# Optimization experiments

Hardware: AMD Instinct MI355X
Metric: run time of the kernel (lower is better)

The kernel has to match this reference:

```python
import jax, jax.numpy as jnp
import numpy as np
import math

N_NODES = 50000
N_EDGES = 800000
IN_FEATS = 128
HID = 64
OUT = 2
D = 2  # num_layers


def calc_thetas(d):
    """Beta-distribution polynomial coefficients (ascending order), matching
    sympy.poly((x/2)**i * (1-x/2)**(d-i) / Beta(i+1, d+1-i)) with inverted coeffs."""
    thetas = []
    for i in range(d + 1):
        p1 = np.zeros(i + 1)
        p1[-1] = 0.5 ** i  # (x/2)^i, ascending coeffs
        p2 = np.array([math.comb(d - i, j) * (-0.5) ** j for j in range(d - i + 1)])  # (1-x/2)^(d-i)
        beta = math.factorial(i) * math.factorial(d - i) / math.factorial(d + 1)
        thetas.append((np.convolve(p1, p2) / beta).tolist())
    return thetas


def poly_branch(h, src, dst, thetas):
    """Run all PolyConv filters on activated features h; concat along feature dim."""
    n = h.shape[0]
    deg = jnp.zeros((n,), h.dtype).at[dst].add(jnp.ones((dst.shape[0],), h.dtype))
    dinv = jnp.clip(deg, 1.0, None) ** -0.5  # D^{-1/2} of in-degrees, clamped min 1
    dinv = dinv[:, None]
    outs = []
    for th in thetas:
        f = h
        acc = th[0] * h
        for k in range(1, len(th)):
            # feat <- feat - D^{-1/2} A D^{-1/2} feat  (copy_u / sum aggregation)
            agg = jax.ops.segment_sum((f * dinv)[src], dst, num_segments=n)
            f = f - agg * dinv
            acc = acc + th[k] * f
        outs.append(acc)
    return jnp.concatenate(outs, axis=-1)


def setup_inputs() -> dict:
    key = jax.random.key(0)
    ks = jax.random.split(key, 12)
    inp = {
        "x": jax.random.normal(ks[0], (N_NODES, IN_FEATS), jnp.float32),
        "sim_x": jax.random.normal(ks[1], (N_NODES, IN_FEATS), jnp.float32),
        "src": jax.random.randint(ks[2], (N_EDGES,), 0, N_NODES, jnp.int32),
        "dst": jax.random.randint(ks[3], (N_EDGES,), 0, N_NODES, jnp.int32),
        "sim_src": jax.random.randint(ks[4], (N_EDGES,), 0, N_NODES, jnp.int32),
        "sim_dst": jax.random.randint(ks[5], (N_EDGES,), 0, N_NODES, jnp.int32),
        "W1_o": jax.random.normal(ks[6], (IN_FEATS, HID), jnp.float32) / np.sqrt(IN_FEATS),
        "b1_o": jnp.zeros((HID,), jnp.float32),
        "W1_s": jax.random.normal(ks[7], (IN_FEATS, HID), jnp.float32) / np.sqrt(IN_FEATS),
        "b1_s": jnp.zeros((HID,), jnp.float32),
        "Wm1": jax.random.normal(ks[8], (HID * (D + 1) * 2, HID), jnp.float32) / np.sqrt(HID * (D + 1) * 2),
        "bm1": jnp.zeros((HID,), jnp.float32),
        "Wm2": jax.random.normal(ks[9], (HID, OUT), jnp.float32) / np.sqrt(HID),
        "bm2": jnp.zeros((OUT,), jnp.float32),
    }
    return inp


def reference(x, sim_x, src, dst, sim_src, sim_dst,
              W1_o, b1_o, W1_s, b1_s, Wm1, bm1, Wm2, bm2):
    thetas_o = calc_thetas(D)
    thetas_s = [[4.0] * (D + 1) for _ in range(D + 1)]  # conv_s uses constant theta=4

    h = jax.nn.relu(x @ W1_o + b1_o)
    h_final = poly_branch(h, src, dst, thetas_o)      # [N, HID*(D+1)]

    sh = jax.nn.relu(sim_x @ W1_s + b1_s)
    sim_h_final = poly_branch(sh, sim_src, sim_dst, thetas_s)

    h_all = jnp.concatenate([h_final, sim_h_final], axis=-1)  # [N, HID*(D+1)*2]
    logits = jax.nn.relu(h_all @ Wm1 + bm1) @ Wm2 + bm2
    return (h_all, logits)
```

## Files before the change

### kernel.cpp

```cpp
#include <hip/hip_runtime.h>
#include <hip/hip_fp16.h>


#define KB_BITS 10
#define KMAX 64
#define PCHUNK 4096
#define PVPT 16

__global__ __launch_bounds__(256) void bhist_kernel(
    const int* __restrict__ dst, const int* __restrict__ sim_dst,
    int* __restrict__ bhist, int E, int Es) {
    __shared__ int h[2 * KMAX];
    int tid = threadIdx.x;
    if (tid < 2 * KMAX) h[tid] = 0;
    __syncthreads();
    int total = E + Es;
    for (int e = blockIdx.x * 256 + tid; e < total; e += gridDim.x * 256) {
        if (e < E) atomicAdd(&h[dst[e] >> KB_BITS], 1);
        else       atomicAdd(&h[KMAX + (sim_dst[e - E] >> KB_BITS)], 1);
    }
    __syncthreads();
    if (tid < 2 * KMAX && h[tid]) atomicAdd(&bhist[tid], h[tid]);
}

__global__ __launch_bounds__(128) void bscan_kernel(
    const int* __restrict__ bhist, int* __restrict__ brow,
    int* __restrict__ gcur) {
    int g = threadIdx.x >> 6, lane = threadIdx.x & 63;
    int v = bhist[g * KMAX + lane];
    int inc = v;
    #pragma unroll
    for (int off = 1; off < 64; off <<= 1) {
        int u = __shfl_up(inc, off);
        if (lane >= off) inc += u;
    }
    int ex = inc - v;
    brow[g * (KMAX + 1) + lane] = ex;
    if (lane == 63) brow[g * (KMAX + 1) + KMAX] = inc;
    gcur[g * KMAX + lane] = ex;
}

__global__ __launch_bounds__(256) void partition_kernel(
    const int* __restrict__ src, const int* __restrict__ dst,
    const int* __restrict__ sim_src, const int* __restrict__ sim_dst,
    int* __restrict__ gcur, unsigned* __restrict__ staged,
    int E, int Es, int nbo) {
    int b = blockIdx.x;
    const int* S; const int* D; int Eg; int goff; unsigned* stg;
    if (b < nbo) { S = src; D = dst; Eg = E; goff = 0; stg = staged; }
    else { b -= nbo; S = sim_src; D = sim_dst; Eg = Es; goff = KMAX; stg = staged + E; }
    int e0 = b * PCHUNK;
    int cnt_blk = Eg - e0; if (cnt_blk > PCHUNK) cnt_blk = PCHUNK;
    __shared__ int hist[KMAX], basep[KMAX], cur[KMAX], gbase[KMAX];
    __shared__ unsigned srt[PCHUNK];
    int tid = threadIdx.x;
    if (tid < KMAX) hist[tid] = 0;
    __syncthreads();
    unsigned full[PVPT];
    #pragma unroll
    for (int i = 0; i < PVPT; ++i) {
        int idx = i * 256 + tid;
        if (idx < cnt_blk) {
            int e = e0 + idx;
            int d = D[e];
            unsigned bk = (unsigned)d >> KB_BITS;
            full[i] = (bk << 26) | ((unsigned)S[e] << KB_BITS) |
                      (unsigned)(d & ((1 << KB_BITS) - 1));
            atomicAdd(&hist[bk], 1);
        } else full[i] = 0xFFFFFFFFu;
    }
    __syncthreads();
    if (tid < 64) {
        int v = hist[tid];
        int inc = v;
        #pragma unroll
        for (int off = 1; off < 64; off <<= 1) {
            int u = __shfl_up(inc, off);
            if (tid >= off) inc += u;
        }
        int ex = inc - v;
        basep[tid] = ex;
        cur[tid] = ex;
        gbase[tid] = v ? atomicAdd(&gcur[goff + tid], v) : 0;
    }
    __syncthreads();
    #pragma unroll
    for (int i = 0; i < PVPT; ++i) {
        unsigned f = full[i];
        if (f != 0xFFFFFFFFu) {
            unsigned bk = f >> 26;
            int slot = atomicAdd(&cur[bk], 1);
            srt[slot] = f;
        }
    }
    __syncthreads();
    for (int slot = tid; slot < cnt_blk; slot += 256) {
        unsigned f = srt[slot];
        unsigned bk = f >> 26;
        int gpos = gbase[bk] + (slot - basep[bk]);
        stg[gpos] = f & 0x3FFFFFFu;
    }
}

__global__ __launch_bounds__(512) void place_kernel(
    const unsigned* __restrict__ staged, const int* __restrict__ brow,
    int* __restrict__ row_o, int* __restrict__ row_s,
    int* __restrict__ esrc_o, int* __restrict__ esrc_s,
    float* __restrict__ dinv, int N, int K, int E) {
    int b = blockIdx.x;
    const unsigned* stg; const int* br; int* row; int* esrc; float* dv;
    if (b < K) { stg = staged; br = brow; row = row_o; esrc = esrc_o; dv = dinv; }
    else { b -= K; stg = staged + E; br = brow + (KMAX + 1); row = row_s; esrc = esrc_s; dv = dinv + N; }
    int node0 = b << KB_BITS;
    int nn = N - node0; if (nn > (1 << KB_BITS)) nn = (1 << KB_BITS);
    int seg0 = br[b], seg1 = br[b + 1];
    __shared__ int ncnt[1 << KB_BITS];
    __shared__ int wsum[8];
    int tid = threadIdx.x;
    for (int i = tid; i < (1 << KB_BITS); i += 512) ncnt[i] = 0;
    __syncthreads();
    for (int j = seg0 + tid; j < seg1; j += 512)
        atomicAdd(&ncnt[stg[j] & ((1 << KB_BITS) - 1)], 1);
    __syncthreads();
    int i0 = tid * 2;
    int v0 = ncnt[i0], v1 = ncnt[i0 + 1];
    int s = v0 + v1;
    int inc = s;
    #pragma unroll
    for (int off = 1; off < 64; off <<= 1) {
        int u = __shfl_up(inc, off);
        if ((tid & 63) >= off) inc += u;
    }
    if ((tid & 63) == 63) wsum[tid >> 6] = inc;
    __syncthreads();
    int wo = 0;
    for (int w = 0; w < (tid >> 6); ++w) wo += wsum[w];
    int ex = seg0 + wo + inc - s;
    if (i0 < nn) {
        row[node0 + i0] = ex;
        dv[node0 + i0] = rsqrtf((float)(v0 > 1 ? v0 : 1));
    }
    if (i0 + 1 < nn) {
        row[node0 + i0 + 1] = ex + v0;
        dv[node0 + i0 + 1] = rsqrtf((float)(v1 > 1 ? v1 : 1));
    }
    if (b == K - 1 && tid == 0) row[N] = br[K];
    __syncthreads();
    ncnt[i0] = ex;
    ncnt[i0 + 1] = ex + v0;
    __syncthreads();
    for (int j = seg0 + tid; j < seg1; j += 512) {
        unsigned f = stg[j];
        int pos = atomicAdd(&ncnt[f & ((1 << KB_BITS) - 1)], 1);
        esrc[pos] = (int)(f >> KB_BITS);
    }
}

__global__ __launch_bounds__(256) void fold_kernel(
    const float* __restrict__ Wm1, float* __restrict__ w1f) {
    int i = blockIdx.x * 256 + threadIdx.x;
    if (i >= 256 * 64) return;
    int k = i >> 6, j = i & 63;
    float v = Wm1[k * 64 + j];
    if (k >= 192) v += Wm1[(k + 64) * 64 + j] + Wm1[(k + 128) * 64 + j];
    w1f[i] = v;
}

__global__ __launch_bounds__(256) void in_gemm2_kernel(
    const float* __restrict__ x, const float* __restrict__ sim_x,
    const float* __restrict__ W1_o, const float* __restrict__ b1_o,
    const float* __restrict__ W1_s, const float* __restrict__ b1_s,
    float* __restrict__ hall, __half* __restrict__ h16_o, __half* __restrict__ h16_s,
    const float* __restrict__ dinv, int n, int nbh, int f16path) {
    int bb = blockIdx.x;
    const float* xin; const float* W; const float* b; __half* h16;
    const float* dinvv; int off;
    if (bb < nbh) { xin = x; W = W1_o; b = b1_o; h16 = h16_o; dinvv = dinv; off = 0; }
    else { bb -= nbh; xin = sim_x; W = W1_s; b = b1_s; h16 = h16_s; dinvv = dinv + n; off = 192; }
    __shared__ float xs[64][132];
    __shared__ float Wf[128][68];
    int tid = threadIdx.x;
    int node0 = bb * 64;
    const float4* wsrc = (const float4*)W;
    for (int i = tid; i < 2048; i += 256)
        *(float4*)&Wf[i >> 4][(i & 15) * 4] = wsrc[i];
    const float4* xsrc = (const float4*)xin;
    for (int i = tid; i < 2048; i += 256) {
        int nl = i >> 5, c = i & 31;
        int node = node0 + nl;
        float4 v = make_float4(0.f, 0.f, 0.f, 0.f);
        if (node < n) v = xsrc[(long)node * 32 + c];
        *(float4*)&xs[nl][c * 4] = v;
    }
    __syncthreads();
    int tx = tid & 15, ty = tid >> 4;
    float acc[4][4] = {};
    #pragma unroll 2
    for (int k = 0; k < 128; k += 4) {
        float4 a[4], bbv[4];
        #pragma unroll
        for (int i = 0; i < 4; ++i) a[i] = *(const float4*)&xs[ty * 4 + i][k];
        #pragma unroll
        for (int j = 0; j < 4; ++j) bbv[j] = *(const float4*)&Wf[k + j][tx * 4];
        #pragma unroll
        for (int i = 0; i < 4; ++i) {
            acc[i][0] = fmaf(a[i].x, bbv[0].x, acc[i][0]);
            acc[i][1] = fmaf(a[i].x, bbv[0].y, acc[i][1]);
            acc[i][2] = fmaf(a[i].x, bbv[0].z, acc[i][2]);
            acc[i][3] = fmaf(a[i].x, bbv[0].w, acc[i][3]);
            acc[i][0] = fmaf(a[i].y, bbv[1].x, acc[i][0]);
            acc[i][1] = fmaf(a[i].y, bbv[1].y, acc[i][1]);
            acc[i][2] = fmaf(a[i].y, bbv[1].z, acc[i][2]);
            acc[i][3] = fmaf(a[i].y, bbv[1].w, acc[i][3]);
            acc[i][0] = fmaf(a[i].z, bbv[2].x, acc[i][0]);
            acc[i][1] = fmaf(a[i].z, bbv[2].y, acc[i][1]);
            acc[i][2] = fmaf(a[i].z, bbv[2].z, acc[i][2]);
            acc[i][3] = fmaf(a[i].z, bbv[2].w, acc[i][3]);
            acc[i][0] = fmaf(a[i].w, bbv[3].x, acc[i][0]);
            acc[i][1] = fmaf(a[i].w, bbv[3].y, acc[i][1]);
            acc[i][2] = fmaf(a[i].w, bbv[3].z, acc[i][2]);
            acc[i][3] = fmaf(a[i].w, bbv[3].w, acc[i][3]);
        }
    }
    float4 bias = *(const float4*)&b[tx * 4];
    #pragma unroll
    for (int i = 0; i < 4; ++i) {
        int node = node0 + ty * 4 + i;
        if (node >= n) break;
        float4 r;
        r.x = fmaxf(acc[i][0] + bias.x, 0.0f);
        r.y = fmaxf(acc[i][1] + bias.y, 0.0f);
        r.z = fmaxf(acc[i][2] + bias.z, 0.0f);
        r.w = fmaxf(acc[i][3] + bias.w, 0.0f);
        if (f16path) {
            float dvn = dinvv[node];
            __half hh[4];
            hh[0] = __float2half_rn(r.x * dvn);
            hh[1] = __float2half_rn(r.y * dvn);
            hh[2] = __float2half_rn(r.z * dvn);
            hh[3] = __float2half_rn(r.w * dvn);
            *(float2*)&h16[(long)node * 64 + tx * 4] = *(float2*)hh;
        } else {
            *(float4*)&hall[(long)node * 384 + off + tx * 4] = r;
        }
    }
}

__global__ __launch_bounds__(256) void hop1_kernel(
    const int* __restrict__ row_o, const int* __restrict__ esrc_o,
    const int* __restrict__ row_s, const int* __restrict__ esrc_s,
    const __half* __restrict__ h16_o, const __half* __restrict__ h16_s,
    __half* __restrict__ g16_o, __half* __restrict__ g16_s,
    int n, int nb) {
    int b = blockIdx.x;
    const int* row; const int* esrc; const __half* h16; __half* g16;
    if (b < nb) { row = row_o; esrc = esrc_o; h16 = h16_o; g16 = g16_o; }
    else { b -= nb; row = row_s; esrc = esrc_s; h16 = h16_s; g16 = g16_s; }
    int d = b * 4 + (threadIdx.x >> 6);
    if (d >= n) return;
    int lane = threadIdx.x & 63;
    int p = row[d], end = row[d + 1];
    int deg = end - p;
    float degf = (float)(deg > 1 ? deg : 1);
    float dd = rsqrtf(degf);
    float h16v = __half2float(h16[(long)d * 64 + lane]);
    float a0 = 0.f, a1 = 0.f, a2 = 0.f, a3 = 0.f;
    for (; p + 16 <= end; p += 16) {
        int ss[16];
        #pragma unroll
        for (int i = 0; i < 16; ++i) ss[i] = esrc[p + i];
        #pragma unroll
        for (int i = 0; i < 16; i += 4) {
            a0 += __half2float(h16[(long)ss[i] * 64 + lane]);
            a1 += __half2float(h16[(long)ss[i + 1] * 64 + lane]);
            a2 += __half2float(h16[(long)ss[i + 2] * 64 + lane]);
            a3 += __half2float(h16[(long)ss[i + 3] * 64 + lane]);
        }
    }
    for (; p + 4 <= end; p += 4) {
        int s0 = esrc[p], s1 = esrc[p + 1], s2 = esrc[p + 2], s3 = esrc[p + 3];
        a0 += __half2float(h16[(long)s0 * 64 + lane]);
        a1 += __half2float(h16[(long)s1 * 64 + lane]);
        a2 += __half2float(h16[(long)s2 * 64 + lane]);
        a3 += __half2float(h16[(long)s3 * 64 + lane]);
    }
    for (; p < end; ++p) {
        int s = esrc[p];
        a0 += __half2float(h16[(long)s * 64 + lane]);
    }
    float acc = (a0 + a1) + (a2 + a3);
    g16[(long)d * 64 + lane] = __float2half_rn(h16v - acc * dd * dd);
}

__global__ __launch_bounds__(256) void hop2_kernel(
    const int* __restrict__ row_o, const int* __restrict__ esrc_o,
    const int* __restrict__ row_s, const int* __restrict__ esrc_s,
    const __half* __restrict__ h16_o, const __half* __restrict__ h16_s,
    const __half* __restrict__ g16_o, const __half* __restrict__ g16_s,
    float* __restrict__ hall, int n, int nb) {
    int b = blockIdx.x;
    int g = (b < nb) ? 0 : 1;
    const int* row; const int* esrc; const __half* h16; const __half* g16;
    if (g == 0) { row = row_o; esrc = esrc_o; h16 = h16_o; g16 = g16_o; }
    else { b -= nb; row = row_s; esrc = esrc_s; h16 = h16_s; g16 = g16_s; }
    int d = b * 4 + (threadIdx.x >> 6);
    if (d >= n) return;
    int lane = threadIdx.x & 63;
    int p = row[d], end = row[d + 1];
    int deg = end - p;
    float degf = (float)(deg > 1 ? deg : 1);
    float dd = rsqrtf(degf);
    float sq = sqrtf(degf);
    float f0 = __half2float(h16[(long)d * 64 + lane]) * sq;
    float f1 = __half2float(g16[(long)d * 64 + lane]) * sq;
    float a0 = 0.f, a1 = 0.f, a2 = 0.f, a3 = 0.f;
    for (; p + 16 <= end; p += 16) {
        int ss[16];
        #pragma unroll
        for (int i = 0; i < 16; ++i) ss[i] = esrc[p + i];
        #pragma unroll
        for (int i = 0; i < 16; i += 4) {
            a0 += __half2float(g16[(long)ss[i] * 64 + lane]);
            a1 += __half2float(g16[(long)ss[i + 1] * 64 + lane]);
            a2 += __half2float(g16[(long)ss[i + 2] * 64 + lane]);
            a3 += __half2float(g16[(long)ss[i + 3] * 64 + lane]);
        }
    }
    for (; p + 4 <= end; p += 4) {
        int s0 = esrc[p], s1 = esrc[p + 1], s2 = esrc[p + 2], s3 = esrc[p + 3];
        a0 += __half2float(g16[(long)s0 * 64 + lane]);
        a1 += __half2float(g16[(long)s1 * 64 + lane]);
        a2 += __half2float(g16[(long)s2 * 64 + lane]);
        a3 += __half2float(g16[(long)s3 * 64 + lane]);
    }
    for (; p < end; ++p) {
        int s = esrc[p];
        a0 += __half2float(g16[(long)s * 64 + lane]);
    }
    float acc = (a0 + a1) + (a2 + a3);
    float f2 = f1 - acc * dd;
    long ob = (long)d * 384 + lane;
    if (g == 0) {
        hall[ob]       = 3.0f * f0 - 3.0f * f1 + 0.75f * f2;
        hall[ob + 64]  = 3.0f * f1 - 1.5f * f2;
        hall[ob + 128] = 0.75f * f2;
    } else {
        float ss = 4.0f * (f0 + f1 + f2);
        hall[ob + 192] = ss; hall[ob + 256] = ss; hall[ob + 320] = ss;
    }
}

__global__ __launch_bounds__(256) void gather2_kernel(
    const int* __restrict__ row_o, const int* __restrict__ esrc_o, const float* __restrict__ dinv_o,
    const int* __restrict__ row_s, const int* __restrict__ esrc_s, const float* __restrict__ dinv_s,
    float* __restrict__ hall, int in_off_o, int in_off_s, int n, int nb) {
    int b = blockIdx.x;
    const int* row; const int* esrc; const float* dinv; int in_off;
    if (b < nb) { row = row_o; esrc = esrc_o; dinv = dinv_o; in_off = in_off_o; }
    else { b -= nb; row = row_s; esrc = esrc_s; dinv = dinv_s; in_off = in_off_s; }
    int d = b * 4 + (threadIdx.x >> 6);
    if (d >= n) return;
    int lane = threadIdx.x & 63;
    int p = row[d], end = row[d + 1];
    const float* fin = hall + in_off;
    float a0 = 0.f, a1 = 0.f, a2 = 0.f, a3 = 0.f;
    for (; p + 4 <= end; p += 4) {
        int s0 = esrc[p], s1 = esrc[p + 1], s2 = esrc[p + 2], s3 = esrc[p + 3];
        a0 = fmaf(fin[(long)s0 * 384 + lane], dinv[s0], a0);
        a1 = fmaf(fin[(long)s1 * 384 + lane], dinv[s1], a1);
        a2 = fmaf(fin[(long)s2 * 384 + lane], dinv[s2], a2);
        a3 = fmaf(fin[(long)s3 * 384 + lane], dinv[s3], a3);
    }
    for (; p < end; ++p) {
        int s = esrc[p];
        a0 = fmaf(fin[(long)s * 384 + lane], dinv[s], a0);
    }
    float acc = (a0 + a1) + (a2 + a3);
    long ob = (long)d * 384 + lane;
    hall[ob + in_off + 64] = fin[ob] - acc * dinv[d];
}

__global__ __launch_bounds__(256) void combine_kernel(float* __restrict__ h, int nf) {
    int i = blockIdx.x * 256 + threadIdx.x;
    if (i >= nf) return;
    long ob = (long)(i >> 6) * 384 + (i & 63);
    float f0v = h[ob], f1v = h[ob + 64], f2v = h[ob + 128];
    h[ob]       = 3.0f * f0v - 3.0f * f1v + 0.75f * f2v;
    h[ob + 64]  = 3.0f * f1v - 1.5f * f2v;
    h[ob + 128] = 0.75f * f2v;
    float ss = 4.0f * (h[ob + 192] + h[ob + 256] + h[ob + 320]);
    h[ob + 192] = ss; h[ob + 256] = ss; h[ob + 320] = ss;
}

__global__ __launch_bounds__(256) void mlp_kernel(
    const float* __restrict__ hall, const float* __restrict__ w1f,
    const float* __restrict__ bm1, const float* __restrict__ Wm2,
    const float* __restrict__ bm2, float* __restrict__ logits, int n) {
    __shared__ float xs[64][132];
    __shared__ float Wf[128][68];
    int tid = threadIdx.x;
    int node0 = blockIdx.x * 64;
    int tx = tid & 15, ty = tid >> 4;
    float acc[4][4] = {};
    const float4* wsrc = (const float4*)w1f;
    const float4* hsrc = (const float4*)hall;
    for (int c = 0; c < 2; ++c) {
        __syncthreads();
        for (int i = tid; i < 2048; i += 256)
            *(float4*)&Wf[i >> 4][(i & 15) * 4] = wsrc[c * 2048 + i];
        for (int i = tid; i < 2048; i += 256) {
            int nl = i >> 5, cc = i & 31;
            int node = node0 + nl;
            float4 v = make_float4(0.f, 0.f, 0.f, 0.f);
            if (node < n) v = hsrc[(long)node * 96 + c * 32 + cc];
            *(float4*)&xs[nl][cc * 4] = v;
        }
        __syncthreads();
        #pragma unroll 2
        for (int k = 0; k < 128; k += 4) {
            float4 a[4], bb[4];
            #pragma unroll
            for (int i = 0; i < 4; ++i) a[i] = *(const float4*)&xs[ty * 4 + i][k];
            #pragma unroll
            for (int j = 0; j < 4; ++j) bb[j] = *(const float4*)&Wf[k + j][tx * 4];
            #pragma unroll
            for (int i = 0; i < 4; ++i) {
                acc[i][0] = fmaf(a[i].x, bb[0].x, acc[i][0]);
                acc[i][1] = fmaf(a[i].x, bb[0].y, acc[i][1]);
                acc[i][2] = fmaf(a[i].x, bb[0].z, acc[i][2]);
                acc[i][3] = fmaf(a[i].x, bb[0].w, acc[i][3]);
                acc[i][0] = fmaf(a[i].y, bb[1].x, acc[i][0]);
                acc[i][1] = fmaf(a[i].y, bb[1].y, acc[i][1]);
                acc[i][2] = fmaf(a[i].y, bb[1].z, acc[i][2]);
                acc[i][3] = fmaf(a[i].y, bb[1].w, acc[i][3]);
                acc[i][0] = fmaf(a[i].z, bb[2].x, acc[i][0]);
                acc[i][1] = fmaf(a[i].z, bb[2].y, acc[i][1]);
                acc[i][2] = fmaf(a[i].z, bb[2].z, acc[i][2]);
                acc[i][3] = fmaf(a[i].z, bb[2].w, acc[i][3]);
                acc[i][0] = fmaf(a[i].w, bb[3].x, acc[i][0]);
                acc[i][1] = fmaf(a[i].w, bb[3].y, acc[i][1]);
                acc[i][2] = fmaf(a[i].w, bb[3].z, acc[i][2]);
                acc[i][3] = fmaf(a[i].w, bb[3].w, acc[i][3]);
            }
        }
    }
    __syncthreads();
    float4 bias = *(const float4*)&bm1[tx * 4];
    #pragma unroll
    for (int i = 0; i < 4; ++i) {
        xs[ty * 4 + i][tx * 4 + 0] = fmaxf(acc[i][0] + bias.x, 0.0f);
        xs[ty * 4 + i][tx * 4 + 1] = fmaxf(acc[i][1] + bias.y, 0.0f);
        xs[ty * 4 + i][tx * 4 + 2] = fmaxf(acc[i][2] + bias.z, 0.0f);
        xs[ty * 4 + i][tx * 4 + 3] = fmaxf(acc[i][3] + bias.w, 0.0f);
    }
    __syncthreads();
    if (tid < 128) {
        int nl = tid >> 1, o = tid & 1;
        int node = node0 + nl;
        if (node < n) {
            float p = bm2[o];
            #pragma unroll 8
            for (int k = 0; k < 64; ++k) p = fmaf(xs[nl][k], Wm2[k * 2 + o], p);
            logits[(long)node * 2 + o] = p;
        }
    }
}

extern "C" void kernel_launch(void* const* d_in, const int* in_sizes, int n_in,
                              void* d_out, int out_size, void* d_ws, size_t ws_size,
                              hipStream_t stream) {
    const float* x     = (const float*)d_in[0];
    const float* sim_x = (const float*)d_in[1];
    const int* src     = (const int*)d_in[2];
    const int* dst     = (const int*)d_in[3];
    const int* sim_src = (const int*)d_in[4];
    const int* sim_dst = (const int*)d_in[5];
    const float* W1_o = (const float*)d_in[6];
    const float* b1_o = (const float*)d_in[7];
    const float* W1_s = (const float*)d_in[8];
    const float* b1_s = (const float*)d_in[9];
    const float* Wm1  = (const float*)d_in[10];
    const float* bm1  = (const float*)d_in[11];
    const float* Wm2  = (const float*)d_in[12];
    const float* bm2  = (const float*)d_in[13];

    const int N  = in_sizes[0] / 128;
    const int E  = in_sizes[2];
    const int Es = in_sizes[4];
    const int NF = N * 64;
    const int K  = (N + (1 << KB_BITS) - 1) >> KB_BITS;

    float* hall = (float*)d_out;
    float* lgt  = hall + (long)N * 384;
    float* dinv = lgt;
    float* dinv_o = dinv;
    float* dinv_s = dinv + N;

    int* row_o  = (int*)d_ws;
    int* row_s  = row_o + (N + 1);
    int* esrc_o = row_s + (N + 1);
    int* esrc_s = esrc_o + E;
    int* bhist  = esrc_s + Es;
    int* brow   = bhist + 2 * KMAX;
    int* gcur   = brow + 2 * (KMAX + 1);
    float* w1f  = (float*)(gcur + 2 * KMAX);
    __half* h16_o = (__half*)(w1f + 256 * 64);
    __half* h16_s = h16_o + (long)N * 64;
    __half* g16_o = h16_s + (long)N * 64;
    __half* g16_s = g16_o + (long)N * 64;
    size_t need_f16 = (size_t)((char*)(g16_s + (long)N * 64) - (char*)d_ws);
    bool f16path = ws_size >= need_f16;
    unsigned* staged = (unsigned*)h16_o;

    int nb4  = (N + 3) / 4;
    int nb64 = (N + 63) / 64;
    int nfb  = (NF + 255) / 256;
    int nbo  = (E + PCHUNK - 1) / PCHUNK;
    int nbs  = (Es + PCHUNK - 1) / PCHUNK;

    hipMemsetAsync(bhist, 0, (size_t)(2 * KMAX) * sizeof(int), stream);
    fold_kernel<<<64, 256, 0, stream>>>(Wm1, w1f);
    bhist_kernel<<<256, 256, 0, stream>>>(dst, sim_dst, bhist, E, Es);
    bscan_kernel<<<1, 128, 0, stream>>>(bhist, brow, gcur);
    partition_kernel<<<nbo + nbs, 256, 0, stream>>>(src, dst, sim_src, sim_dst,
                                                    gcur, staged, E, Es, nbo);
    place_kernel<<<2 * K, 512, 0, stream>>>(staged, brow, row_o, row_s,
                                            esrc_o, esrc_s, dinv, N, K, E);

    in_gemm2_kernel<<<2 * nb64, 256, 0, stream>>>(x, sim_x, W1_o, b1_o, W1_s, b1_s,
                                                  hall, h16_o, h16_s, dinv, N, nb64,
                                                  f16path ? 1 : 0);

    if (f16path) {
        hop1_kernel<<<2 * nb4, 256, 0, stream>>>(row_o, esrc_o, row_s, esrc_s,
                                                 h16_o, h16_s, g16_o, g16_s, N, nb4);
        hop2_kernel<<<2 * nb4, 256, 0, stream>>>(row_o, esrc_o, row_s, esrc_s,
                                                 h16_o, h16_s, g16_o, g16_s,
                                                 hall, N, nb4);
    } else {
        gather2_kernel<<<2 * nb4, 256, 0, stream>>>(row_o, esrc_o, dinv_o,
                                                    row_s, esrc_s, dinv_s,
                                                    hall, 0, 192, N, nb4);
        gather2_kernel<<<2 * nb4, 256, 0, stream>>>(row_o, esrc_o, dinv_o,
                                                    row_s, esrc_s, dinv_s,
                                                    hall, 64, 256, N, nb4);
        combine_kernel<<<nfb, 256, 0, stream>>>(hall, NF);
    }

    mlp_kernel<<<nb64, 256, 0, stream>>>(hall, w1f, bm1, Wm2, bm2, lgt, N);
}
```

Before: 375.0 us.

## Pad CSR neighbor lists to multiples of eight with a zero sentinel node

Each node's neighbor list is padded to a multiple of 8 entries that point at an extra all-zero sentinel row. This lets the hop kernels run mostly in unrolled 8- and 16-wide gather blocks instead of scalar tail loops. Row end pointers come from a separate pend array, and the hop kernels now read the precomputed dinv instead of recomputing rsqrt. The bhist memset is folded into fold_kernel, at the cost of extra edge storage, sentinel writes, and more gathers of the zero row.

```diff
diff --git a/kernel.cpp b/kernel.cpp
--- a/kernel.cpp
+++ b/kernel.cpp
@@ -6,6 +6,7 @@
 #define KMAX 64
 #define PCHUNK 4096
 #define PVPT 16
+#define PADMAX 7168
 
 __global__ __launch_bounds__(256) void bhist_kernel(
     const int* __restrict__ dst, const int* __restrict__ sim_dst,
@@ -105,15 +106,17 @@
 __global__ __launch_bounds__(512) void place_kernel(
     const unsigned* __restrict__ staged, const int* __restrict__ brow,
     int* __restrict__ row_o, int* __restrict__ row_s,
+    int* __restrict__ pend_o, int* __restrict__ pend_s,
     int* __restrict__ esrc_o, int* __restrict__ esrc_s,
-    float* __restrict__ dinv, int N, int K, int E) {
+    float* __restrict__ dinv, int N, int K, int E, int pad) {
     int b = blockIdx.x;
-    const unsigned* stg; const int* br; int* row; int* esrc; float* dv;
-    if (b < K) { stg = staged; br = brow; row = row_o; esrc = esrc_o; dv = dinv; }
-    else { b -= K; stg = staged + E; br = brow + (KMAX + 1); row = row_s; esrc = esrc_s; dv = dinv + N; }
+    const unsigned* stg; const int* br; int* row; int* pend; int* esrc; float* dv;
+    if (b < K) { stg = staged; br = brow; row = row_o; pend = pend_o; esrc = esrc_o; dv = dinv; }
+    else { b -= K; stg = staged + E; br = brow + (KMAX + 1); row = row_s; pend = pend_s; esrc = esrc_s; dv = dinv + N; }
     int node0 = b << KB_BITS;
     int nn = N - node0; if (nn > (1 << KB_BITS)) nn = (1 << KB_BITS);
     int seg0 = br[b], seg1 = br[b + 1];
+    int base = pad ? (seg0 + b * PADMAX) : seg0;
     __shared__ int ncnt[1 << KB_BITS];
     __shared__ int wsum[8];
     int tid = threadIdx.x;
@@ -124,7 +127,9 @@
     __syncthreads();
     int i0 = tid * 2;
     int v0 = ncnt[i0], v1 = ncnt[i0 + 1];
-    int s = v0 + v1;
+    int p0 = pad ? ((v0 + 7) & ~7) : v0;
+    int p1 = pad ? ((v1 + 7) & ~7) : v1;
+    int s = p0 + p1;
     int inc = s;
     #pragma unroll
     for (int off = 1; off < 64; off <<= 1) {
@@ -135,19 +140,24 @@
     __syncthreads();
     int wo = 0;
     for (int w = 0; w < (tid >> 6); ++w) wo += wsum[w];
-    int ex = seg0 + wo + inc - s;
+    int ex = base + wo + inc - s;
     if (i0 < nn) {
         row[node0 + i0] = ex;
+        pend[node0 + i0] = ex + p0;
         dv[node0 + i0] = rsqrtf((float)(v0 > 1 ? v0 : 1));
+        for (int q = ex + v0; q < ex + p0; ++q) esrc[q] = N;
     }
     if (i0 + 1 < nn) {
-        row[node0 + i0 + 1] = ex + v0;
+        int ex2 = ex + p0;
+        row[node0 + i0 + 1] = ex2;
+        pend[node0 + i0 + 1] = ex2 + p1;
         dv[node0 + i0 + 1] = rsqrtf((float)(v1 > 1 ? v1 : 1));
-    }
-    if (b == K - 1 && tid == 0) row[N] = br[K];
+        for (int q = ex2 + v1; q < ex2 + p1; ++q) esrc[q] = N;
+    }
+    if (!pad && b == K - 1 && tid == 0) row[N] = br[K];
     __syncthreads();
     ncnt[i0] = ex;
-    ncnt[i0 + 1] = ex + v0;
+    ncnt[i0 + 1] = ex + p0;
     __syncthreads();
     for (int j = seg0 + tid; j < seg1; j += 512) {
         unsigned f = stg[j];
@@ -157,8 +167,10 @@
 }
 
 __global__ __launch_bounds__(256) void fold_kernel(
-    const float* __restrict__ Wm1, float* __restrict__ w1f) {
+    const float* __restrict__ Wm1, float* __restrict__ w1f,
+    int* __restrict__ bhist) {
     int i = blockIdx.x * 256 + threadIdx.x;
+    if (blockIdx.x == 0 && threadIdx.x < 2 * KMAX) bhist[threadIdx.x] = 0;
     if (i >= 256 * 64) return;
     int k = i >> 6, j = i & 63;
     float v = Wm1[k * 64 + j];
@@ -171,12 +183,22 @@
     const float* __restrict__ W1_o, const float* __restrict__ b1_o,
     const float* __restrict__ W1_s, const float* __restrict__ b1_s,
     float* __restrict__ hall, __half* __restrict__ h16_o, __half* __restrict__ h16_s,
-    const float* __restrict__ dinv, int n, int nbh, int f16path) {
+    __half* __restrict__ g16_o, __half* __restrict__ g16_s,
+    const float* __restrict__ dinv, int n, int nbh, int f16path, int pad) {
     int bb = blockIdx.x;
     const float* xin; const float* W; const float* b; __half* h16;
     const float* dinvv; int off;
     if (bb < nbh) { xin = x; W = W1_o; b = b1_o; h16 = h16_o; dinvv = dinv; off = 0; }
     else { bb -= nbh; xin = sim_x; W = W1_s; b = b1_s; h16 = h16_s; dinvv = dinv + n; off = 192; }
+    if (pad && threadIdx.x < 64) {
+        if (blockIdx.x == 0) {
+            h16_o[(long)n * 64 + threadIdx.x] = __float2half_rn(0.f);
+            g16_o[(long)n * 64 + threadIdx.x] = __float2half_rn(0.f);
+        } else if (blockIdx.x == nbh) {
+            h16_s[(long)n * 64 + threadIdx.x] = __float2half_rn(0.f);
+            g16_s[(long)n * 64 + threadIdx.x] = __float2half_rn(0.f);
+        }
+    }
     __shared__ float xs[64][132];
     __shared__ float Wf[128][68];
     int tid = threadIdx.x;
@@ -247,22 +269,23 @@
 }
 
 __global__ __launch_bounds__(256) void hop1_kernel(
-    const int* __restrict__ row_o, const int* __restrict__ esrc_o,
-    const int* __restrict__ row_s, const int* __restrict__ esrc_s,
+    const int* __restrict__ row_o, const int* __restrict__ pend_o,
+    const int* __restrict__ esrc_o, const float* __restrict__ dinv_o,
+    const int* __restrict__ row_s, const int* __restrict__ pend_s,
+    const int* __restrict__ esrc_s, const float* __restrict__ dinv_s,
     const __half* __restrict__ h16_o, const __half* __restrict__ h16_s,
     __half* __restrict__ g16_o, __half* __restrict__ g16_s,
     int n, int nb) {
     int b = blockIdx.x;
-    const int* row; const int* esrc; const __half* h16; __half* g16;
-    if (b < nb) { row = row_o; esrc = esrc_o; h16 = h16_o; g16 = g16_o; }
-    else { b -= nb; row = row_s; esrc = esrc_s; h16 = h16_s; g16 = g16_s; }
+    const int* row; const int* pend; const int* esrc; const float* dinv;
+    const __half* h16; __half* g16;
+    if (b < nb) { row = row_o; pend = pend_o; esrc = esrc_o; dinv = dinv_o; h16 = h16_o; g16 = g16_o; }
+    else { b -= nb; row = row_s; pend = pend_s; esrc = esrc_s; dinv = dinv_s; h16 = h16_s; g16 = g16_s; }
     int d = b * 4 + (threadIdx.x >> 6);
     if (d >= n) return;
     int lane = threadIdx.x & 63;
-    int p = row[d], end = row[d + 1];
-    int deg = end - p;
-    float degf = (float)(deg > 1 ? deg : 1);
-    float dd = rsqrtf(degf);
+    int p = row[d], end = pend[d];
+    float dd = dinv[d];
     float h16v = __half2float(h16[(long)d * 64 + lane]);
     float a0 = 0.f, a1 = 0.f, a2 = 0.f, a3 = 0.f;
     for (; p + 16 <= end; p += 16) {
@@ -276,6 +299,19 @@
             a2 += __half2float(h16[(long)ss[i + 2] * 64 + lane]);
             a3 += __half2float(h16[(long)ss[i + 3] * 64 + lane]);
         }
+    }
+    if (p + 8 <= end) {
+        int ss[8];
+        #pragma unroll
+        for (int i = 0; i < 8; ++i) ss[i] = esrc[p + i];
+        #pragma unroll
+        for (int i = 0; i < 8; i += 4) {
+            a0 += __half2float(h16[(long)ss[i] * 64 + lane]);
+            a1 += __half2float(h16[(long)ss[i + 1] * 64 + lane]);
+            a2 += __half2float(h16[(long)ss[i + 2] * 64 + lane]);
+            a3 += __half2float(h16[(long)ss[i + 3] * 64 + lane]);
+        }
+        p += 8;
     }
     for (; p + 4 <= end; p += 4) {
         int s0 = esrc[p], s1 = esrc[p + 1], s2 = esrc[p + 2], s3 = esrc[p + 3];
@@ -293,24 +329,25 @@
 }
 
 __global__ __launch_bounds__(256) void hop2_kernel(
-    const int* __restrict__ row_o, const int* __restrict__ esrc_o,
-    const int* __restrict__ row_s, const int* __restrict__ esrc_s,
+    const int* __restrict__ row_o, const int* __restrict__ pend_o,
+    const int* __restrict__ esrc_o, const float* __restrict__ dinv_o,
+    const int* __restrict__ row_s, const int* __restrict__ pend_s,
+    const int* __restrict__ esrc_s, const float* __restrict__ dinv_s,
     const __half* __restrict__ h16_o, const __half* __restrict__ h16_s,
     const __half* __restrict__ g16_o, const __half* __restrict__ g16_s,
     float* __restrict__ hall, int n, int nb) {
     int b = blockIdx.x;
     int g = (b < nb) ? 0 : 1;
-    const int* row; const int* esrc; const __half* h16; const __half* g16;
-    if (g == 0) { row = row_o; esrc = esrc_o; h16 = h16_o; g16 = g16_o; }
-    else { b -= nb; row = row_s; esrc = esrc_s; h16 = h16_s; g16 = g16_s; }
+    const int* row; const int* pend; const int* esrc; const float* dinv;
+    const __half* h16; const __half* g16;
+    if (g == 0) { row = row_o; pend = pend_o; esrc = esrc_o; dinv = dinv_o; h16 = h16_o; g16 = g16_o; }
+    else { b -= nb; row = row_s; pend = pend_s; esrc = esrc_s; dinv = dinv_s; h16 = h16_s; g16 = g16_s; }
     int d = b * 4 + (threadIdx.x >> 6);
     if (d >= n) return;
     int lane = threadIdx.x & 63;
-    int p = row[d], end = row[d + 1];
-    int deg = end - p;
-    float degf = (float)(deg > 1 ? deg : 1);
-    float dd = rsqrtf(degf);
-    float sq = sqrtf(degf);
+    int p = row[d], end = pend[d];
+    float dd = dinv[d];
+    float sq = 1.0f / dd;
     float f0 = __half2float(h16[(long)d * 64 + lane]) * sq;
     float f1 = __half2float(g16[(long)d * 64 + lane]) * sq;
     float a0 = 0.f, a1 = 0.f, a2 = 0.f, a3 = 0.f;
@@ -325,6 +362,19 @@
             a2 += __half2float(g16[(long)ss[i + 2] * 64 + lane]);
             a3 += __half2float(g16[(long)ss[i + 3] * 64 + lane]);
         }
+    }
+    if (p + 8 <= end) {
+        int ss[8];
+        #pragma unroll
+        for (int i = 0; i < 8; ++i) ss[i] = esrc[p + i];
+        #pragma unroll
+        for (int i = 0; i < 8; i += 4) {
+            a0 += __half2float(g16[(long)ss[i] * 64 + lane]);
+            a1 += __half2float(g16[(long)ss[i + 1] * 64 + lane]);
+            a2 += __half2float(g16[(long)ss[i + 2] * 64 + lane]);
+            a3 += __half2float(g16[(long)ss[i + 3] * 64 + lane]);
+        }
+        p += 8;
     }
     for (; p + 4 <= end; p += 4) {
         int s0 = esrc[p], s1 = esrc[p + 1], s2 = esrc[p + 2], s3 = esrc[p + 3];
@@ -498,19 +548,40 @@
 
     int* row_o  = (int*)d_ws;
     int* row_s  = row_o + (N + 1);
-    int* esrc_o = row_s + (N + 1);
-    int* esrc_s = esrc_o + E;
-    int* bhist  = esrc_s + Es;
+    int* pend_o = row_s + (N + 1);
+    int* pend_s = pend_o + N;
+    int* esrc_o = pend_s + N;
+    long esz_pad = (long)E + (long)K * PADMAX;
+    long esz_pad_s = (long)Es + (long)K * PADMAX;
+
+    int* esrc_sA = esrc_o + esz_pad;
+    int* bhistA  = esrc_sA + esz_pad_s;
+    int* esrc_sB = esrc_o + E;
+    int* bhistB  = esrc_sB + Es;
+
+    auto layout_tail = [&](int* bh) -> char* {
+        int* br = bh + 2 * KMAX;
+        int* gc = br + 2 * (KMAX + 1);
+        float* wf = (float*)(gc + 2 * KMAX);
+        __half* h = (__half*)(wf + 256 * 64);
+        return (char*)(h + 4 * (long)(N + 1) * 64);
+    };
+    bool padA = (size_t)(layout_tail(bhistA) - (char*)d_ws) <= ws_size;
+    int* esrc_s = padA ? esrc_sA : esrc_sB;
+    int* bhist  = padA ? bhistA : bhistB;
     int* brow   = bhist + 2 * KMAX;
     int* gcur   = brow + 2 * (KMAX + 1);
     float* w1f  = (float*)(gcur + 2 * KMAX);
     __half* h16_o = (__half*)(w1f + 256 * 64);
-    __half* h16_s = h16_o + (long)N * 64;
-    __half* g16_o = h16_s + (long)N * 64;
-    __half* g16_s = g16_o + (long)N * 64;
-    size_t need_f16 = (size_t)((char*)(g16_s + (long)N * 64) - (char*)d_ws);
-    bool f16path = ws_size >= need_f16;
+    __half* h16_s = h16_o + (long)(N + 1) * 64;
+    __half* g16_o = h16_s + (long)(N + 1) * 64;
+    __half* g16_s = g16_o + (long)(N + 1) * 64;
+    bool f16path = padA ||
+        ((size_t)(layout_tail(bhistB) - (char*)d_ws) <= ws_size);
+    int pad = padA ? 1 : 0;
     unsigned* staged = (unsigned*)h16_o;
+    const int* pend_o_use = pad ? pend_o : (row_o + 1);
+    const int* pend_s_use = pad ? pend_s : (row_s + 1);
 
     int nb4  = (N + 3) / 4;
     int nb64 = (N + 63) / 64;
@@ -518,23 +589,25 @@
     int nbo  = (E + PCHUNK - 1) / PCHUNK;
     int nbs  = (Es + PCHUNK - 1) / PCHUNK;
 
-    hipMemsetAsync(bhist, 0, (size_t)(2 * KMAX) * sizeof(int), stream);
-    fold_kernel<<<64, 256, 0, stream>>>(Wm1, w1f);
+    fold_kernel<<<64, 256, 0, stream>>>(Wm1, w1f, bhist);
     bhist_kernel<<<256, 256, 0, stream>>>(dst, sim_dst, bhist, E, Es);
     bscan_kernel<<<1, 128, 0, stream>>>(bhist, brow, gcur);
     partition_kernel<<<nbo + nbs, 256, 0, stream>>>(src, dst, sim_src, sim_dst,
                                                     gcur, staged, E, Es, nbo);
     place_kernel<<<2 * K, 512, 0, stream>>>(staged, brow, row_o, row_s,
-                                            esrc_o, esrc_s, dinv, N, K, E);
+                                            pend_o, pend_s, esrc_o, esrc_s,
+                                            dinv, N, K, E, pad);
 
     in_gemm2_kernel<<<2 * nb64, 256, 0, stream>>>(x, sim_x, W1_o, b1_o, W1_s, b1_s,
-                                                  hall, h16_o, h16_s, dinv, N, nb64,
-                                                  f16path ? 1 : 0);
+                                                  hall, h16_o, h16_s, g16_o, g16_s,
+                                                  dinv, N, nb64, f16path ? 1 : 0, pad);
 
     if (f16path) {
-        hop1_kernel<<<2 * nb4, 256, 0, stream>>>(row_o, esrc_o, row_s, esrc_s,
+        hop1_kernel<<<2 * nb4, 256, 0, stream>>>(row_o, pend_o_use, esrc_o, dinv_o,
+                                                 row_s, pend_s_use, esrc_s, dinv_s,
                                                  h16_o, h16_s, g16_o, g16_s, N, nb4);
-        hop2_kernel<<<2 * nb4, 256, 0, stream>>>(row_o, esrc_o, row_s, esrc_s,
+        hop2_kernel<<<2 * nb4, 256, 0, stream>>>(row_o, pend_o_use, esrc_o, dinv_o,
+                                                 row_s, pend_s_use, esrc_s, dinv_s,
                                                  h16_o, h16_s, g16_o, g16_s,
                                                  hall, N, nb4);
     } else {
```

Measured after the change: 351.7 us. -6.2%, faster.
